# Performance work log

Measured on AMD Instinct MI355X. Metric: run time of the kernel, lower is better.

## Reference

```python
import jax, jax.numpy as jnp
import numpy as np

N_QUBITS = 10
DIM = 1 << N_QUBITS  # 1024

# Constant QFT matrix (PennyLane convention: F[j,k] = w^{jk}/sqrt(N), w = exp(2*pi*i/N),
# wire 0 = most significant bit). Symmetric, so state @ F == F @ state per sample.
_jk = (np.outer(np.arange(DIM), np.arange(DIM)) % DIM).astype(np.float64)
QFT_MAT = jnp.asarray((np.exp(2j * np.pi * _jk / DIM) / np.sqrt(DIM)).astype(np.complex64))


def _apply_1q(state, U, q):
    """Apply 2x2 gate U to wire q (wire 0 = MSB). state: [B, DIM] complex."""
    B = state.shape[0]
    left, right = 1 << q, 1 << (N_QUBITS - 1 - q)
    s = state.reshape(B, left, 2, right)
    s = jnp.einsum('ij,bajc->baic', U, s)
    return s.reshape(B, DIM)


def _apply_cnot(state, c, t):
    """CNOT with control c, target t (wire 0 = MSB)."""
    B = state.shape[0]
    a, b = (c, t) if c < t else (t, c)
    s = state.reshape(B, 1 << a, 2, 1 << (b - a - 1), 2, 1 << (N_QUBITS - 1 - b))
    ctrl_ax, tgt_ax = (2, 4) if c < t else (4, 2)
    s0 = jax.lax.index_in_dim(s, 0, ctrl_ax, keepdims=False)
    s1 = jax.lax.index_in_dim(s, 1, ctrl_ax, keepdims=False)
    ta = tgt_ax - 1 if tgt_ax > ctrl_ax else tgt_ax  # target axis after squeezing ctrl
    s1 = jnp.flip(s1, axis=ta)  # X on target when control == 1
    s = jnp.stack([s0, s1], axis=ctrl_ax)
    return s.reshape(B, DIM)


def _rx(t):
    c = jnp.cos(t / 2).astype(jnp.complex64)
    s = (-1j * jnp.sin(t / 2)).astype(jnp.complex64)
    return jnp.stack([jnp.stack([c, s]), jnp.stack([s, c])])


def _ry(t):
    c = jnp.cos(t / 2).astype(jnp.complex64)
    s = jnp.sin(t / 2).astype(jnp.complex64)
    return jnp.stack([jnp.stack([c, -s]), jnp.stack([s, c])])


def _rz(t):
    e = jnp.exp(-0.5j * t.astype(jnp.complex64))
    z = jnp.zeros((), jnp.complex64)
    return jnp.stack([jnp.stack([e, z]), jnp.stack([z, jnp.conj(e)])])


def _forward(x, weights):
    B = x.shape[0]
    # Pad/truncate is a no-op here (x already [B, DIM]); normalize as in the module.
    nrm = jnp.linalg.norm(x, axis=-1, keepdims=True)
    xn = x / jnp.maximum(nrm, 1e-8)
    state = xn.astype(jnp.complex64)  # AmplitudeEmbedding (already unit-norm)
    for q in range(N_QUBITS):
        state = _apply_1q(state, _rx(weights[q, 0]), q)
    for q in range(N_QUBITS):
        state = _apply_1q(state, _ry(weights[q, 1]), q)
    for q in range(N_QUBITS):
        state = _apply_1q(state, _rz(weights[q, 2]), q)
    for q in range(N_QUBITS):
        state = _apply_cnot(state, q, (q + 1) % N_QUBITS)
    for q in range(N_QUBITS):
        state = _apply_1q(state, _ry(weights[q, 3]), q)
    state = state @ QFT_MAT  # QFT (symmetric matrix)
    ex, ey, ez = [], [], []
    for q in range(N_QUBITS):
        s = state.reshape(B, 1 << q, 2, 1 << (N_QUBITS - 1 - q))
        s0, s1 = s[:, :, 0, :], s[:, :, 1, :]
        cross = jnp.sum(jnp.conj(s0) * s1, axis=(1, 2))
        ex.append(2.0 * jnp.real(cross))                # <X_q>
        ey.append(2.0 * jnp.imag(cross))                # <Y_q>
        ez.append(jnp.sum(jnp.abs(s0) ** 2 - jnp.abs(s1) ** 2, axis=(1, 2)))  # <Z_q>
    return jnp.stack(ex + ey + ez, axis=1).astype(jnp.float32)  # [B, 3*N_QUBITS]


def setup_inputs() -> dict:
    key = jax.random.key(0)
    kx, kw = jax.random.split(key)
    x = jax.random.normal(kx, (8192, 1024), dtype=jnp.float32)
    weights = jax.random.normal(kw, (10, 4), dtype=jnp.float32) * 0.01
    return {"x": x, "weights": weights}


def reference(x, weights):
    return _forward(x, weights)
```

## Files before the change

kernel.cpp:

```cpp
#include <hip/hip_runtime.h>


typedef _Float16 half2_t __attribute__((ext_vector_type(2)));

__device__ __forceinline__ unsigned pk16(float a, float b) {
    half2_t h; h[0] = (_Float16)a; h[1] = (_Float16)b;
    return __builtin_bit_cast(unsigned, h);
}
__device__ __forceinline__ float2 up16(unsigned u) {
    half2_t h = __builtin_bit_cast(half2_t, u);
    return make_float2((float)h[0], (float)h[1]);
}

__device__ __forceinline__ float wred(float v) {
    v += __shfl_xor(v, 1);
    v += __shfl_xor(v, 2);
    v += __shfl_xor(v, 4);
    v += __shfl_xor(v, 8);
    v += __shfl_xor(v, 16);
    v += __shfl_xor(v, 32);
    return v;
}

__device__ __forceinline__ int cnotrev(int k) {
    int m = (int)(__brev((unsigned)k) >> 22);
    #pragma unroll
    for (int q = 9; q >= 0; --q) {
        const int pc = (q == 9) ? 0 : 9 - q;
        const int pt = (q == 9) ? 9 : 8 - q;
        m ^= ((m >> pc) & 1) << pt;
    }
    return m;
}

__global__ __launch_bounds__(256) void fused_kernel(const float* __restrict__ w,
                                                    const float* __restrict__ x,
                                                    float* __restrict__ out)
{
    __shared__ float uu[10][8];
    __shared__ float ryc[10], rys[10];
    __shared__ __align__(16) unsigned scr[4][1024];
    const int tid = threadIdx.x;
    const int wv = tid >> 6, l = tid & 63;
    const int row = blockIdx.x * 4 + wv;
    unsigned* bw = scr[wv];

    if (tid < 10) {
        float t0 = w[tid*4 + 0] * 0.5f, t1 = w[tid*4 + 1] * 0.5f;
        float t2 = w[tid*4 + 2] * 0.5f, t3 = w[tid*4 + 3] * 0.5f;
        float s0, c0, s1, c1, s2, c2, s3, c3;
        __sincosf(t0, &s0, &c0);
        __sincosf(t1, &s1, &c1);
        __sincosf(t2, &s2, &c2);
        __sincosf(t3, &s3, &c3);
        uu[tid][0] =  c2*c1*c0 + s2*s1*s0;
        uu[tid][1] =  c2*s1*s0 - s2*c1*c0;
        uu[tid][2] = -(c2*s1*c0 + s2*c1*s0);
        uu[tid][3] =  s2*s1*c0 - c2*c1*s0;
        uu[tid][4] =  c2*s1*c0 + s2*c1*s0;
        uu[tid][5] =  s2*s1*c0 - c2*c1*s0;
        uu[tid][6] =  c2*c1*c0 + s2*s1*s0;
        uu[tid][7] =  s2*c1*c0 - c2*s1*s0;
        ryc[tid] = c3;
        rys[tid] = s3;
    }
    __syncthreads();

    const float* xr = x + (size_t)row * 1024 + l * 16;
    float4 v0 = ((const float4*)xr)[0];
    float4 v1 = ((const float4*)xr)[1];
    float4 v2 = ((const float4*)xr)[2];
    float4 v3 = ((const float4*)xr)[3];
    float ss = v0.x*v0.x + v0.y*v0.y + v0.z*v0.z + v0.w*v0.w
             + v1.x*v1.x + v1.y*v1.y + v1.z*v1.z + v1.w*v1.w
             + v2.x*v2.x + v2.y*v2.y + v2.z*v2.z + v2.w*v2.w
             + v3.x*v3.x + v3.y*v3.y + v3.z*v3.z + v3.w*v3.w;
    ss = wred(ss);
    const float scale = 0.03125f / fmaxf(sqrtf(ss), 1e-8f);

    float2 c[16];
    c[0]  = make_float2(v0.x*scale, 0.f); c[1]  = make_float2(v0.y*scale, 0.f);
    c[2]  = make_float2(v0.z*scale, 0.f); c[3]  = make_float2(v0.w*scale, 0.f);
    c[4]  = make_float2(v1.x*scale, 0.f); c[5]  = make_float2(v1.y*scale, 0.f);
    c[6]  = make_float2(v1.z*scale, 0.f); c[7]  = make_float2(v1.w*scale, 0.f);
    c[8]  = make_float2(v2.x*scale, 0.f); c[9]  = make_float2(v2.y*scale, 0.f);
    c[10] = make_float2(v2.z*scale, 0.f); c[11] = make_float2(v2.w*scale, 0.f);
    c[12] = make_float2(v3.x*scale, 0.f); c[13] = make_float2(v3.y*scale, 0.f);
    c[14] = make_float2(v3.z*scale, 0.f); c[15] = make_float2(v3.w*scale, 0.f);

    #pragma unroll
    for (int p = 0; p < 4; ++p) {
        const float* U = uu[9 - p];
        const float u00r = U[0], u00i = U[1], u01r = U[2], u01i = U[3];
        const float u10r = U[4], u10i = U[5], u11r = U[6], u11i = U[7];
        const int m = 1 << p;
        #pragma unroll
        for (int i = 0; i < 16; ++i) {
            if (i & m) continue;
            const int j = i | m;
            const float ar = c[i].x, ai = c[i].y, br = c[j].x, bi = c[j].y;
            c[i].x = u00r*ar - u00i*ai + u01r*br - u01i*bi;
            c[i].y = u00r*ai + u00i*ar + u01r*bi + u01i*br;
            c[j].x = u10r*ar - u10i*ai + u11r*br - u11i*bi;
            c[j].y = u10r*ai + u10i*ar + u11r*bi + u11i*br;
        }
    }
    #pragma unroll
    for (int e = 0; e < 6; ++e) {
        const float* U = uu[5 - e];
        const int mybit = (l >> e) & 1;
        const float car = mybit ? U[6] : U[0];
        const float cai = mybit ? U[7] : U[1];
        const float cbr = mybit ? U[4] : U[2];
        const float cbi = mybit ? U[5] : U[3];
        #pragma unroll
        for (int i = 0; i < 16; ++i) {
            const float fr = __shfl_xor(c[i].x, 1 << e);
            const float fi = __shfl_xor(c[i].y, 1 << e);
            const float ar = c[i].x, ai = c[i].y;
            c[i].x = car*ar - cai*ai + cbr*fr - cbi*fi;
            c[i].y = car*ai + cai*ar + cbr*fi + cbi*fr;
        }
    }

    #pragma unroll
    for (int j = 0; j < 8; ++j) {
        const int su = l*8 + (j ^ (l & 7));
        uint2 pv;
        pv.x = pk16(c[2*j].x,     c[2*j].y);
        pv.y = pk16(c[2*j + 1].x, c[2*j + 1].y);
        ((uint2*)bw)[su] = pv;
    }
    const int mb = cnotrev(l << 4);
    #pragma unroll
    for (int i = 0; i < 16; ++i) {
        const int m = mb ^ cnotrev(i);
        const int lm = m >> 4, um = (m >> 1) & 7, lo = m & 1;
        c[i] = up16(bw[(lm*8 + (um ^ (lm & 7)))*2 + lo]);
    }

    #pragma unroll
    for (int p = 0; p < 4; ++p) {
        const float cc = ryc[p], sv = rys[p];
        const int m = 1 << p;
        #pragma unroll
        for (int i = 0; i < 16; ++i) {
            if (i & m) continue;
            const int j = i | m;
            const float ar = c[i].x, ai = c[i].y, br = c[j].x, bi = c[j].y;
            c[i].x = cc*ar - sv*br;  c[i].y = cc*ai - sv*bi;
            c[j].x = sv*ar + cc*br;  c[j].y = sv*ai + cc*bi;
        }
    }
    #pragma unroll
    for (int e = 0; e < 6; ++e) {
        const float cc = ryc[4 + e], sv = rys[4 + e];
        const int mybit = (l >> e) & 1;
        const float sel = mybit ? sv : -sv;
        #pragma unroll
        for (int i = 0; i < 16; ++i) {
            const float fr = __shfl_xor(c[i].x, 1 << e);
            const float fi = __shfl_xor(c[i].y, 1 << e);
            c[i].x = cc*c[i].x + sel*fr;
            c[i].y = cc*c[i].y + sel*fi;
        }
    }

    {
        const float TC8[8] = { 1.f,  0.92387953f,  0.70710678f,  0.38268343f,
                               0.f, -0.38268343f, -0.70710678f, -0.92387953f };
        const float TS8[8] = { 0.f,  0.38268343f,  0.70710678f,  0.92387953f,
                               1.f,  0.92387953f,  0.70710678f,  0.38268343f };
        #pragma unroll
        for (int st = 1; st <= 4; ++st) {
            const int hf = 1 << (st - 1);
            #pragma unroll
            for (int i = 0; i < 16; ++i) {
                if (i & hf) continue;
                const int j = i | hf;
                const int tix = (i & (hf - 1)) << (4 - st);
                const float cwv = TC8[tix], swv = TS8[tix];
                const float tr = cwv*c[j].x - swv*c[j].y;
                const float ti = cwv*c[j].y + swv*c[j].x;
                const float ur = c[i].x, ui = c[i].y;
                c[i].x = ur + tr; c[i].y = ui + ti;
                c[j].x = ur - tr; c[j].y = ui - ti;
            }
        }
    }
    {
        const float CT[6][16] = {
          { 1.f,0.98078528f,0.92387953f,0.83146961f,0.70710678f,0.55557023f,0.38268343f,0.19509032f,
            0.f,-0.19509032f,-0.38268343f,-0.55557023f,-0.70710678f,-0.83146961f,-0.92387953f,-0.98078528f },
          { 1.f,0.99518473f,0.98078528f,0.95694034f,0.92387953f,0.88192126f,0.83146961f,0.77301045f,
            0.70710678f,0.63439328f,0.55557023f,0.47139674f,0.38268343f,0.29028468f,0.19509032f,0.09801714f },
          { 1.f,0.99879546f,0.99518473f,0.98917651f,0.98078528f,0.97003125f,0.95694034f,0.94154407f,
            0.92387953f,0.90398929f,0.88192126f,0.85772861f,0.83146961f,0.80320753f,0.77301045f,0.74095113f },
          { 1.f,0.99969882f,0.99879546f,0.99729046f,0.99518473f,0.99247953f,0.98917651f,0.98527764f,
            0.98078528f,0.97570213f,0.97003125f,0.96377607f,0.95694034f,0.94952818f,0.94154407f,0.93299280f },
          { 1.f,0.99992470f,0.99969882f,0.99932238f,0.99879546f,0.99811811f,0.99729046f,0.99631261f,
            0.99518473f,0.99390697f,0.99247953f,0.99090264f,0.98917651f,0.98730142f,0.98527764f,0.98310549f },
          { 1.f,0.99998118f,0.99992470f,0.99983058f,0.99969882f,0.99952942f,0.99932238f,0.99907773f,
            0.99879546f,0.99847559f,0.99811811f,0.99772307f,0.99729046f,0.99682030f,0.99631261f,0.99576742f } };
        const float ST[6][16] = {
          { 0.f,0.19509032f,0.38268343f,0.55557023f,0.70710678f,0.83146961f,0.92387953f,0.98078528f,
            1.f,0.98078528f,0.92387953f,0.83146961f,0.70710678f,0.55557023f,0.38268343f,0.19509032f },
          { 0.f,0.09801714f,0.19509032f,0.29028468f,0.38268343f,0.47139674f,0.55557023f,0.63439328f,
            0.70710678f,0.77301045f,0.83146961f,0.88192126f,0.92387953f,0.95694034f,0.98078528f,0.99518473f },
          { 0.f,0.04906767f,0.09801714f,0.14673047f,0.19509032f,0.24298018f,0.29028468f,0.33688985f,
            0.38268343f,0.42755509f,0.47139674f,0.51410274f,0.55557023f,0.59569930f,0.63439328f,0.67155895f },
          { 0.f,0.02454123f,0.04906767f,0.07356456f,0.09801714f,0.12241068f,0.14673047f,0.17096189f,
            0.19509032f,0.21910124f,0.24298018f,0.26671276f,0.29028468f,0.31368174f,0.33688985f,0.35989504f },
          { 0.f,0.01227154f,0.02454123f,0.03680722f,0.04906767f,0.06132074f,0.07356456f,0.08579731f,
            0.09801714f,0.11022221f,0.12241068f,0.13458071f,0.14673047f,0.15885814f,0.17096189f,0.18303989f },
          { 0.f,0.00613588f,0.01227154f,0.01840673f,0.02454123f,0.03067480f,0.03680722f,0.04293826f,
            0.04906767f,0.05519524f,0.06132074f,0.06744392f,0.07356456f,0.07968244f,0.08579731f,0.09190896f } };
        #pragma unroll
        for (int e2 = 0; e2 < 6; ++e2) {
            const int st = 5 + e2;
            const float astep = 6.28318530717958647f / (float)(1 << st);
            const int mybit = (l >> e2) & 1;
            const float sel = mybit ? -1.f : 1.f;
            float cb, sb;
            __sincosf(astep * 16.0f * (float)(l & ((1 << e2) - 1)), &sb, &cb);
            #pragma unroll
            for (int i = 0; i < 16; ++i) {
                const float cw = cb*CT[e2][i] - sb*ST[e2][i];
                const float sw = sb*CT[e2][i] + cb*ST[e2][i];
                const float pr = cw*c[i].x - sw*c[i].y;
                const float pi = cw*c[i].y + sw*c[i].x;
                const float vr = mybit ? pr : c[i].x;
                const float vi = mybit ? pi : c[i].y;
                const float fr = __shfl_xor(vr, 1 << e2);
                const float fi = __shfl_xor(vi, 1 << e2);
                c[i].x = fmaf(sel, vr, fr);
                c[i].y = fmaf(sel, vi, fi);
            }
        }
    }

    #pragma unroll
    for (int j = 0; j < 8; ++j) {
        const int su = l*8 + (j ^ (l & 7));
        uint2 pv;
        pv.x = pk16(c[2*j].x,     c[2*j].y);
        pv.y = pk16(c[2*j + 1].x, c[2*j + 1].y);
        ((uint2*)bw)[su] = pv;
    }

    float P2s = 0.f;
    #pragma unroll
    for (int i = 0; i < 16; ++i)
        P2s += c[i].x*c[i].x + c[i].y*c[i].y;

    float outv = 0.f;

    #pragma unroll
    for (int p = 0; p < 4; ++p) {
        const int m = 1 << p;
        const int q = 9 - p;
        float rr = 0.f, ii = 0.f, zz = 0.f;
        #pragma unroll
        for (int i = 0; i < 16; ++i) {
            if (i & m) continue;
            const int j = i | m;
            rr += c[i].x*c[j].x + c[i].y*c[j].y;
            ii += c[i].x*c[j].y - c[i].y*c[j].x;
            zz += (c[i].x*c[i].x + c[i].y*c[i].y) - (c[j].x*c[j].x + c[j].y*c[j].y);
        }
        rr = wred(rr);
        ii = wred(ii);
        zz = wred(zz);
        outv = (l == q)      ? 2.f*rr : outv;
        outv = (l == 10 + q) ? 2.f*ii : outv;
        outv = (l == 20 + q) ? zz     : outv;
    }

    #pragma unroll
    for (int e = 0; e < 6; ++e) {
        const int q = 5 - e;
        const int part = l ^ (1 << e);
        const int mybit = (l >> e) & 1;
        const float sgn = mybit ? -1.f : 1.f;
        const int j0 = mybit ? 4 : 0;
        float rr = 0.f, ii = 0.f;
        #pragma unroll
        for (int j = 0; j < 4; ++j) {
            const int su = part*8 + ((j0 + j) ^ (part & 7));
            const uint2 d = ((const uint2*)bw)[su];
            const float2 f01 = up16(d.x);
            const float2 f23 = up16(d.y);
            const float2 a0 = c[2*j],     a1 = c[2*j + 1];
            const float2 b0 = c[2*j + 8], b1 = c[2*j + 9];
            const float m0x = mybit ? b0.x : a0.x;
            const float m0y = mybit ? b0.y : a0.y;
            const float m1x = mybit ? b1.x : a1.x;
            const float m1y = mybit ? b1.y : a1.y;
            rr += m0x*f01.x + m0y*f01.y;
            ii += m0x*f01.y - m0y*f01.x;
            rr += m1x*f23.x + m1y*f23.y;
            ii += m1x*f23.y - m1y*f23.x;
        }
        const float rr_s = wred(rr);
        const float ii_s = wred(sgn * ii);
        const float zz_s = wred(sgn * P2s);
        outv = (l == q)      ? 2.f*rr_s : outv;
        outv = (l == 10 + q) ? 2.f*ii_s : outv;
        outv = (l == 20 + q) ? zz_s     : outv;
    }

    if (l < 30)
        out[(size_t)row * 30 + l] = outv;
}

extern "C" void kernel_launch(void* const* d_in, const int* in_sizes, int n_in,
                              void* d_out, int out_size, void* d_ws, size_t ws_size,
                              hipStream_t stream) {
    const float* x = (const float*)d_in[0];
    const float* w = (const float*)d_in[1];
    float* out = (float*)d_out;
    (void)d_ws; (void)ws_size;

    fused_kernel<<<2048, 256, 0, stream>>>(w, x, out);
}
```

Measured before the change: 158.4 us.

## Process two state-vector rows per wavefront to amortize setup and raise ILP

Each wavefront now carries two batch rows through the whole circuit, holding two 16-amplitude register arrays and interleaving their gate, shuffle and FFT work. The grid is halved and the shared scratch per wave doubles to hold both rows' fp16 copies. The goal is more independent instructions to hide shuffle and LDS latency, and to amortize the per-block gate-matrix setup and twiddle computation over twice as many rows. The cost is roughly doubled register use and shared memory, which may reduce occupancy, plus fewer blocks in the grid.

```diff
diff --git a/kernel.cpp b/kernel.cpp
--- a/kernel.cpp
+++ b/kernel.cpp
@@ -39,10 +39,10 @@
 {
     __shared__ float uu[10][8];
     __shared__ float ryc[10], rys[10];
-    __shared__ __align__(16) unsigned scr[4][1024];
+    __shared__ __align__(16) unsigned scr[4][2048];
     const int tid = threadIdx.x;
     const int wv = tid >> 6, l = tid & 63;
-    const int row = blockIdx.x * 4 + wv;
+    const int row0 = blockIdx.x * 8 + wv * 2;
     unsigned* bw = scr[wv];
 
     if (tid < 10) {
@@ -66,27 +66,29 @@
     }
     __syncthreads();
 
-    const float* xr = x + (size_t)row * 1024 + l * 16;
-    float4 v0 = ((const float4*)xr)[0];
-    float4 v1 = ((const float4*)xr)[1];
-    float4 v2 = ((const float4*)xr)[2];
-    float4 v3 = ((const float4*)xr)[3];
-    float ss = v0.x*v0.x + v0.y*v0.y + v0.z*v0.z + v0.w*v0.w
-             + v1.x*v1.x + v1.y*v1.y + v1.z*v1.z + v1.w*v1.w
-             + v2.x*v2.x + v2.y*v2.y + v2.z*v2.z + v2.w*v2.w
-             + v3.x*v3.x + v3.y*v3.y + v3.z*v3.z + v3.w*v3.w;
-    ss = wred(ss);
-    const float scale = 0.03125f / fmaxf(sqrtf(ss), 1e-8f);
-
-    float2 c[16];
-    c[0]  = make_float2(v0.x*scale, 0.f); c[1]  = make_float2(v0.y*scale, 0.f);
-    c[2]  = make_float2(v0.z*scale, 0.f); c[3]  = make_float2(v0.w*scale, 0.f);
-    c[4]  = make_float2(v1.x*scale, 0.f); c[5]  = make_float2(v1.y*scale, 0.f);
-    c[6]  = make_float2(v1.z*scale, 0.f); c[7]  = make_float2(v1.w*scale, 0.f);
-    c[8]  = make_float2(v2.x*scale, 0.f); c[9]  = make_float2(v2.y*scale, 0.f);
-    c[10] = make_float2(v2.z*scale, 0.f); c[11] = make_float2(v2.w*scale, 0.f);
-    c[12] = make_float2(v3.x*scale, 0.f); c[13] = make_float2(v3.y*scale, 0.f);
-    c[14] = make_float2(v3.z*scale, 0.f); c[15] = make_float2(v3.w*scale, 0.f);
+    float2 c[2][16];
+    #pragma unroll
+    for (int r = 0; r < 2; ++r) {
+        const float* xr = x + (size_t)(row0 + r) * 1024 + l * 16;
+        float4 v0 = ((const float4*)xr)[0];
+        float4 v1 = ((const float4*)xr)[1];
+        float4 v2 = ((const float4*)xr)[2];
+        float4 v3 = ((const float4*)xr)[3];
+        float ss = v0.x*v0.x + v0.y*v0.y + v0.z*v0.z + v0.w*v0.w
+                 + v1.x*v1.x + v1.y*v1.y + v1.z*v1.z + v1.w*v1.w
+                 + v2.x*v2.x + v2.y*v2.y + v2.z*v2.z + v2.w*v2.w
+                 + v3.x*v3.x + v3.y*v3.y + v3.z*v3.z + v3.w*v3.w;
+        ss = wred(ss);
+        const float scale = 0.03125f / fmaxf(sqrtf(ss), 1e-8f);
+        c[r][0]  = make_float2(v0.x*scale, 0.f); c[r][1]  = make_float2(v0.y*scale, 0.f);
+        c[r][2]  = make_float2(v0.z*scale, 0.f); c[r][3]  = make_float2(v0.w*scale, 0.f);
+        c[r][4]  = make_float2(v1.x*scale, 0.f); c[r][5]  = make_float2(v1.y*scale, 0.f);
+        c[r][6]  = make_float2(v1.z*scale, 0.f); c[r][7]  = make_float2(v1.w*scale, 0.f);
+        c[r][8]  = make_float2(v2.x*scale, 0.f); c[r][9]  = make_float2(v2.y*scale, 0.f);
+        c[r][10] = make_float2(v2.z*scale, 0.f); c[r][11] = make_float2(v2.w*scale, 0.f);
+        c[r][12] = make_float2(v3.x*scale, 0.f); c[r][13] = make_float2(v3.y*scale, 0.f);
+        c[r][14] = make_float2(v3.z*scale, 0.f); c[r][15] = make_float2(v3.w*scale, 0.f);
+    }
 
     #pragma unroll
     for (int p = 0; p < 4; ++p) {
@@ -98,11 +100,15 @@
         for (int i = 0; i < 16; ++i) {
             if (i & m) continue;
             const int j = i | m;
-            const float ar = c[i].x, ai = c[i].y, br = c[j].x, bi = c[j].y;
-            c[i].x = u00r*ar - u00i*ai + u01r*br - u01i*bi;
-            c[i].y = u00r*ai + u00i*ar + u01r*bi + u01i*br;
-            c[j].x = u10r*ar - u10i*ai + u11r*br - u11i*bi;
-            c[j].y = u10r*ai + u10i*ar + u11r*bi + u11i*br;
+            #pragma unroll
+            for (int r = 0; r < 2; ++r) {
+                const float ar = c[r][i].x, ai = c[r][i].y;
+                const float br = c[r][j].x, bi = c[r][j].y;
+                c[r][i].x = u00r*ar - u00i*ai + u01r*br - u01i*bi;
+                c[r][i].y = u00r*ai + u00i*ar + u01r*bi + u01i*br;
+                c[r][j].x = u10r*ar - u10i*ai + u11r*br - u11i*bi;
+                c[r][j].y = u10r*ai + u10i*ar + u11r*bi + u11i*br;
+            }
         }
     }
     #pragma unroll
@@ -115,28 +121,36 @@
         const float cbi = mybit ? U[5] : U[3];
         #pragma unroll
         for (int i = 0; i < 16; ++i) {
-            const float fr = __shfl_xor(c[i].x, 1 << e);
-            const float fi = __shfl_xor(c[i].y, 1 << e);
-            const float ar = c[i].x, ai = c[i].y;
-            c[i].x = car*ar - cai*ai + cbr*fr - cbi*fi;
-            c[i].y = car*ai + cai*ar + cbr*fi + cbi*fr;
-        }
-    }
-
-    #pragma unroll
-    for (int j = 0; j < 8; ++j) {
-        const int su = l*8 + (j ^ (l & 7));
-        uint2 pv;
-        pv.x = pk16(c[2*j].x,     c[2*j].y);
-        pv.y = pk16(c[2*j + 1].x, c[2*j + 1].y);
-        ((uint2*)bw)[su] = pv;
+            #pragma unroll
+            for (int r = 0; r < 2; ++r) {
+                const float fr = __shfl_xor(c[r][i].x, 1 << e);
+                const float fi = __shfl_xor(c[r][i].y, 1 << e);
+                const float ar = c[r][i].x, ai = c[r][i].y;
+                c[r][i].x = car*ar - cai*ai + cbr*fr - cbi*fi;
+                c[r][i].y = car*ai + cai*ar + cbr*fi + cbi*fr;
+            }
+        }
+    }
+
+    #pragma unroll
+    for (int r = 0; r < 2; ++r) {
+        #pragma unroll
+        for (int j = 0; j < 8; ++j) {
+            const int su = r*512 + l*8 + (j ^ (l & 7));
+            uint2 pv;
+            pv.x = pk16(c[r][2*j].x,     c[r][2*j].y);
+            pv.y = pk16(c[r][2*j + 1].x, c[r][2*j + 1].y);
+            ((uint2*)bw)[su] = pv;
+        }
     }
     const int mb = cnotrev(l << 4);
     #pragma unroll
     for (int i = 0; i < 16; ++i) {
         const int m = mb ^ cnotrev(i);
         const int lm = m >> 4, um = (m >> 1) & 7, lo = m & 1;
-        c[i] = up16(bw[(lm*8 + (um ^ (lm & 7)))*2 + lo]);
+        const int base = (lm*8 + (um ^ (lm & 7)))*2 + lo;
+        c[0][i] = up16(bw[base]);
+        c[1][i] = up16(bw[1024 + base]);
     }
 
     #pragma unroll
@@ -147,9 +161,13 @@
         for (int i = 0; i < 16; ++i) {
             if (i & m) continue;
             const int j = i | m;
-            const float ar = c[i].x, ai = c[i].y, br = c[j].x, bi = c[j].y;
-            c[i].x = cc*ar - sv*br;  c[i].y = cc*ai - sv*bi;
-            c[j].x = sv*ar + cc*br;  c[j].y = sv*ai + cc*bi;
+            #pragma unroll
+            for (int r = 0; r < 2; ++r) {
+                const float ar = c[r][i].x, ai = c[r][i].y;
+                const float br = c[r][j].x, bi = c[r][j].y;
+                c[r][i].x = cc*ar - sv*br;  c[r][i].y = cc*ai - sv*bi;
+                c[r][j].x = sv*ar + cc*br;  c[r][j].y = sv*ai + cc*bi;
+            }
         }
     }
     #pragma unroll
@@ -159,10 +177,13 @@
         const float sel = mybit ? sv : -sv;
         #pragma unroll
         for (int i = 0; i < 16; ++i) {
-            const float fr = __shfl_xor(c[i].x, 1 << e);
-            const float fi = __shfl_xor(c[i].y, 1 << e);
-            c[i].x = cc*c[i].x + sel*fr;
-            c[i].y = cc*c[i].y + sel*fi;
+            #pragma unroll
+            for (int r = 0; r < 2; ++r) {
+                const float fr = __shfl_xor(c[r][i].x, 1 << e);
+                const float fi = __shfl_xor(c[r][i].y, 1 << e);
+                c[r][i].x = cc*c[r][i].x + sel*fr;
+                c[r][i].y = cc*c[r][i].y + sel*fi;
+            }
         }
     }
 
@@ -180,11 +201,14 @@
                 const int j = i | hf;
                 const int tix = (i & (hf - 1)) << (4 - st);
                 const float cwv = TC8[tix], swv = TS8[tix];
-                const float tr = cwv*c[j].x - swv*c[j].y;
-                const float ti = cwv*c[j].y + swv*c[j].x;
-                const float ur = c[i].x, ui = c[i].y;
-                c[i].x = ur + tr; c[i].y = ui + ti;
-                c[j].x = ur - tr; c[j].y = ui - ti;
+                #pragma unroll
+                for (int r = 0; r < 2; ++r) {
+                    const float tr = cwv*c[r][j].x - swv*c[r][j].y;
+                    const float ti = cwv*c[r][j].y + swv*c[r][j].x;
+                    const float ur = c[r][i].x, ui = c[r][i].y;
+                    c[r][i].x = ur + tr; c[r][i].y = ui + ti;
+                    c[r][j].x = ur - tr; c[r][j].y = ui - ti;
+                }
             }
         }
     }
@@ -227,53 +251,65 @@
             for (int i = 0; i < 16; ++i) {
                 const float cw = cb*CT[e2][i] - sb*ST[e2][i];
                 const float sw = sb*CT[e2][i] + cb*ST[e2][i];
-                const float pr = cw*c[i].x - sw*c[i].y;
-                const float pi = cw*c[i].y + sw*c[i].x;
-                const float vr = mybit ? pr : c[i].x;
-                const float vi = mybit ? pi : c[i].y;
-                const float fr = __shfl_xor(vr, 1 << e2);
-                const float fi = __shfl_xor(vi, 1 << e2);
-                c[i].x = fmaf(sel, vr, fr);
-                c[i].y = fmaf(sel, vi, fi);
-            }
-        }
-    }
-
-    #pragma unroll
-    for (int j = 0; j < 8; ++j) {
-        const int su = l*8 + (j ^ (l & 7));
-        uint2 pv;
-        pv.x = pk16(c[2*j].x,     c[2*j].y);
-        pv.y = pk16(c[2*j + 1].x, c[2*j + 1].y);
-        ((uint2*)bw)[su] = pv;
-    }
-
-    float P2s = 0.f;
-    #pragma unroll
-    for (int i = 0; i < 16; ++i)
-        P2s += c[i].x*c[i].x + c[i].y*c[i].y;
-
-    float outv = 0.f;
+                #pragma unroll
+                for (int r = 0; r < 2; ++r) {
+                    const float pr = cw*c[r][i].x - sw*c[r][i].y;
+                    const float pi = cw*c[r][i].y + sw*c[r][i].x;
+                    const float vr = mybit ? pr : c[r][i].x;
+                    const float vi = mybit ? pi : c[r][i].y;
+                    const float fr = __shfl_xor(vr, 1 << e2);
+                    const float fi = __shfl_xor(vi, 1 << e2);
+                    c[r][i].x = fmaf(sel, vr, fr);
+                    c[r][i].y = fmaf(sel, vi, fi);
+                }
+            }
+        }
+    }
+
+    #pragma unroll
+    for (int r = 0; r < 2; ++r) {
+        #pragma unroll
+        for (int j = 0; j < 8; ++j) {
+            const int su = r*512 + l*8 + (j ^ (l & 7));
+            uint2 pv;
+            pv.x = pk16(c[r][2*j].x,     c[r][2*j].y);
+            pv.y = pk16(c[r][2*j + 1].x, c[r][2*j + 1].y);
+            ((uint2*)bw)[su] = pv;
+        }
+    }
+
+    float P2s[2] = {0.f, 0.f};
+    #pragma unroll
+    for (int i = 0; i < 16; ++i) {
+        P2s[0] += c[0][i].x*c[0][i].x + c[0][i].y*c[0][i].y;
+        P2s[1] += c[1][i].x*c[1][i].x + c[1][i].y*c[1][i].y;
+    }
+
+    float outv[2] = {0.f, 0.f};
 
     #pragma unroll
     for (int p = 0; p < 4; ++p) {
         const int m = 1 << p;
         const int q = 9 - p;
-        float rr = 0.f, ii = 0.f, zz = 0.f;
-        #pragma unroll
-        for (int i = 0; i < 16; ++i) {
-            if (i & m) continue;
-            const int j = i | m;
-            rr += c[i].x*c[j].x + c[i].y*c[j].y;
-            ii += c[i].x*c[j].y - c[i].y*c[j].x;
-            zz += (c[i].x*c[i].x + c[i].y*c[i].y) - (c[j].x*c[j].x + c[j].y*c[j].y);
-        }
-        rr = wred(rr);
-        ii = wred(ii);
-        zz = wred(zz);
-        outv = (l == q)      ? 2.f*rr : outv;
-        outv = (l == 10 + q) ? 2.f*ii : outv;
-        outv = (l == 20 + q) ? zz     : outv;
+        #pragma unroll
+        for (int r = 0; r < 2; ++r) {
+            float rr = 0.f, ii = 0.f, zz = 0.f;
+            #pragma unroll
+            for (int i = 0; i < 16; ++i) {
+                if (i & m) continue;
+                const int j = i | m;
+                rr += c[r][i].x*c[r][j].x + c[r][i].y*c[r][j].y;
+                ii += c[r][i].x*c[r][j].y - c[r][i].y*c[r][j].x;
+                zz += (c[r][i].x*c[r][i].x + c[r][i].y*c[r][i].y)
+                    - (c[r][j].x*c[r][j].x + c[r][j].y*c[r][j].y);
+            }
+            rr = wred(rr);
+            ii = wred(ii);
+            zz = wred(zz);
+            outv[r] = (l == q)      ? 2.f*rr : outv[r];
+            outv[r] = (l == 10 + q) ? 2.f*ii : outv[r];
+            outv[r] = (l == 20 + q) ? zz     : outv[r];
+        }
     }
 
     #pragma unroll
@@ -283,34 +319,39 @@
         const int mybit = (l >> e) & 1;
         const float sgn = mybit ? -1.f : 1.f;
         const int j0 = mybit ? 4 : 0;
-        float rr = 0.f, ii = 0.f;
-        #pragma unroll
-        for (int j = 0; j < 4; ++j) {
-            const int su = part*8 + ((j0 + j) ^ (part & 7));
-            const uint2 d = ((const uint2*)bw)[su];
-            const float2 f01 = up16(d.x);
-            const float2 f23 = up16(d.y);
-            const float2 a0 = c[2*j],     a1 = c[2*j + 1];
-            const float2 b0 = c[2*j + 8], b1 = c[2*j + 9];
-            const float m0x = mybit ? b0.x : a0.x;
-            const float m0y = mybit ? b0.y : a0.y;
-            const float m1x = mybit ? b1.x : a1.x;
-            const float m1y = mybit ? b1.y : a1.y;
-            rr += m0x*f01.x + m0y*f01.y;
-            ii += m0x*f01.y - m0y*f01.x;
-            rr += m1x*f23.x + m1y*f23.y;
-            ii += m1x*f23.y - m1y*f23.x;
-        }
-        const float rr_s = wred(rr);
-        const float ii_s = wred(sgn * ii);
-        const float zz_s = wred(sgn * P2s);
-        outv = (l == q)      ? 2.f*rr_s : outv;
-        outv = (l == 10 + q) ? 2.f*ii_s : outv;
-        outv = (l == 20 + q) ? zz_s     : outv;
-    }
-
-    if (l < 30)
-        out[(size_t)row * 30 + l] = outv;
+        #pragma unroll
+        for (int r = 0; r < 2; ++r) {
+            float rr = 0.f, ii = 0.f;
+            #pragma unroll
+            for (int j = 0; j < 4; ++j) {
+                const int su = r*512 + part*8 + ((j0 + j) ^ (part & 7));
+                const uint2 d = ((const uint2*)bw)[su];
+                const float2 f01 = up16(d.x);
+                const float2 f23 = up16(d.y);
+                const float2 a0 = c[r][2*j],     a1 = c[r][2*j + 1];
+                const float2 b0 = c[r][2*j + 8], b1 = c[r][2*j + 9];
+                const float m0x = mybit ? b0.x : a0.x;
+                const float m0y = mybit ? b0.y : a0.y;
+                const float m1x = mybit ? b1.x : a1.x;
+                const float m1y = mybit ? b1.y : a1.y;
+                rr += m0x*f01.x + m0y*f01.y;
+                ii += m0x*f01.y - m0y*f01.x;
+                rr += m1x*f23.x + m1y*f23.y;
+                ii += m1x*f23.y - m1y*f23.x;
+            }
+            const float rr_s = wred(rr);
+            const float ii_s = wred(sgn * ii);
+            const float zz_s = wred(sgn * P2s[r]);
+            outv[r] = (l == q)      ? 2.f*rr_s : outv[r];
+            outv[r] = (l == 10 + q) ? 2.f*ii_s : outv[r];
+            outv[r] = (l == 20 + q) ? zz_s     : outv[r];
+        }
+    }
+
+    if (l < 30) {
+        out[(size_t)(row0 + 0) * 30 + l] = outv[0];
+        out[(size_t)(row0 + 1) * 30 + l] = outv[1];
+    }
 }
 
 extern "C" void kernel_launch(void* const* d_in, const int* in_sizes, int n_in,
@@ -321,5 +362,5 @@
     float* out = (float*)d_out;
     (void)d_ws; (void)ws_size;
 
-    fused_kernel<<<2048, 256, 0, stream>>>(w, x, out);
-}
+    fused_kernel<<<1024, 256, 0, stream>>>(w, x, out);
+}
```

Result: slower. 214.4 us (+35.3%).
